# Kernel tuning notes

Measured on AMD Instinct MI355X. Metric: run time of the kernel, lower is better.

Reference implementation:

```python
import jax, jax.numpy as jnp
import numpy as np

DIM = 512
HEADS = 8
DIM_HEAD = 64
SEG = 64        # total_segment_len = segment_len + num_longterm_mem_tokens = 64
PM = 4          # num_persist_mem_tokens


def setup_inputs() -> dict:
    key = jax.random.key(0)
    ks = jax.random.split(key, 5)
    Bv, Hv, Wv = 4, 128, 128
    seq = jax.random.normal(ks[0], (Bv, Hv * Wv, DIM), jnp.float32)
    norm_w = jnp.ones((DIM,), jnp.float32)          # RMSNorm gamma
    s = DIM ** -0.5
    Wq = jax.random.normal(ks[1], (DIM, HEADS * DIM_HEAD), jnp.float32) * s
    Wkv = jax.random.normal(ks[2], (DIM, 2 * HEADS * DIM_HEAD), jnp.float32) * s
    Wo = jax.random.normal(ks[3], (HEADS * DIM_HEAD, DIM), jnp.float32) * s
    # torch inits task_memory to zeros; use small random values for a nontrivial baseline
    task_memory = jax.random.normal(ks[4], (2, HEADS, PM, DIM_HEAD), jnp.float32) * 0.02
    return {"seq": seq, "B": Bv, "H": Hv, "W": Wv, "idx": 0,
            "norm_w": norm_w, "Wq": Wq, "Wkv": Wkv, "Wo": Wo,
            "task_memory": task_memory}


def _rope(x):
    # lucidrains rotary-embedding-torch style: interleaved pairs, theta=10000
    n, d = x.shape[-2], x.shape[-1]
    inv = 1.0 / (10000.0 ** (jnp.arange(0, d, 2, dtype=jnp.float32) / d))
    fr = jnp.arange(n, dtype=jnp.float32)[:, None] * inv      # (n, d/2)
    fr = jnp.repeat(fr, 2, axis=-1)                            # (n, d) interleaved repeat
    cos, sin = jnp.cos(fr), jnp.sin(fr)
    xp = x.reshape(*x.shape[:-1], d // 2, 2)
    rot = jnp.stack((-xp[..., 1], xp[..., 0]), axis=-1).reshape(x.shape)
    return x * cos + rot * sin


def reference(seq, B, H, W, idx, norm_w, Wq, Wkv, Wo, task_memory):
    heads, dh, seg = HEADS, DIM_HEAD, SEG
    N = H * W                      # W % seg == 0 -> segmentation pad is a no-op reshape
    x = seq.reshape(B, N, DIM)
    # RMSNorm
    eps = jnp.finfo(x.dtype).eps
    x = x * jax.lax.rsqrt(jnp.mean(x * x, axis=-1, keepdims=True) + eps) * norm_w
    # cross-attention batch-half reversal trick
    x_rev = jnp.concatenate([x[B // 2:], x[:B // 2]], axis=0)
    q = x @ Wq                                  # (B, N, h*d)
    k, v = jnp.split(x_rev @ Wkv, 2, axis=-1)
    def split_heads(t):
        return t.reshape(B, N, heads, dh).transpose(0, 2, 1, 3)   # (B, h, N, d)
    q, k, v = map(split_heads, (q, k, v))
    orig_v = v
    q, k = _rope(q), _rope(k)
    # segment into windows of length seg: 'b h (w n) d -> (b w) h n d'
    w = N // seg
    def to_win(t):
        return t.reshape(B, heads, w, seg, dh).transpose(0, 2, 1, 3, 4).reshape(B * w, heads, seg, dh)
    q, k, v = map(to_win, (q, k, v))
    # prepend persistent (task) memory tokens to k/v
    pm = task_memory.shape[2]
    tmk = jnp.broadcast_to(task_memory[0], (B * w, heads, pm, dh))
    tmv = jnp.broadcast_to(task_memory[1], (B * w, heads, pm, dh))
    k = jnp.concatenate([tmk, k], axis=-2)
    v = jnp.concatenate([tmv, v], axis=-2)
    # attention within each window (non-causal, no mask)
    scores = jnp.einsum('bhid,bhjd->bhij', q, k) * (dh ** -0.5)
    attn = jax.nn.softmax(scores, axis=-1)
    out = jnp.einsum('bhij,bhjd->bhid', attn, v)
    out = out.transpose(0, 2, 1, 3).reshape(B * w, seg, heads * dh)
    out = out @ Wo
    out = out.reshape(B, w * seg, DIM)          # inverse_segment is identity (no pad)
    return out, orig_v
```

## Files before the change

kernel.cpp:

```cpp
#include <hip/hip_runtime.h>

typedef unsigned short u16;
typedef unsigned int u32;
typedef __attribute__((ext_vector_type(8))) short short8;
typedef __attribute__((ext_vector_type(4))) float f32x4;

__device__ __forceinline__ float b2f(u32 u) {
    union { u32 i; float f; } x; x.i = u << 16; return x.f;
}
__device__ __forceinline__ u16 f2b(float f) {
    union { float f; u32 i; } x; x.f = f;
    u32 u = x.i;
    u += 0x7fffu + ((u >> 16) & 1u);
    return (u16)(u >> 16);
}
__device__ __forceinline__ u32 pack2(float a, float b) {
    return (u32)f2b(a) | ((u32)f2b(b) << 16);
}
__device__ __forceinline__ void gl_lds16(const u16* g, u16* l) {
    __builtin_amdgcn_global_load_lds(
        (const __attribute__((address_space(1))) u32*)g,
        (__attribute__((address_space(3))) u32*)l, 16, 0, 0);
}

__global__ void rope_tab(float* __restrict__ cosT, float* __restrict__ sinT) {
    int idx = blockIdx.x * 256 + threadIdx.x;
    int n = idx >> 5, i = idx & 31;
    float inv = exp2f(-(float)i * 0.41524101186091903f);
    float ang = (float)n * inv;
    float s, c;
    sincosf(ang, &s, &c);
    cosT[idx] = c; sinT[idx] = s;
}

__global__ void conv_w(const float* __restrict__ Wq, const float* __restrict__ Wkv,
                       const float* __restrict__ Wo,
                       u16* __restrict__ wqkvT, u16* __restrict__ woT) {
    int idx = blockIdx.x * 256 + threadIdx.x;
    if (idx < 786432) {
        int n = idx >> 9, k = idx & 511;
        float v = (n < 512) ? Wq[k * 512 + n] : Wkv[k * 1024 + (n - 512)];
        wqkvT[idx] = f2b(v);
    } else {
        int j = idx - 786432;
        int n = j >> 9, k = j & 511;
        woT[j] = f2b(Wo[k * 512 + n]);
    }
}

__launch_bounds__(256)
__global__ void rmsnorm_k(const float* __restrict__ x, const float* __restrict__ g,
                          u16* __restrict__ xn) {
    int row  = blockIdx.x * 4 + (threadIdx.x >> 6);
    int lane = threadIdx.x & 63;
    const float4* p = (const float4*)(x + (size_t)row * 512);
    float4 a = p[lane * 2], b = p[lane * 2 + 1];
    float ss = a.x*a.x + a.y*a.y + a.z*a.z + a.w*a.w
             + b.x*b.x + b.y*b.y + b.z*b.z + b.w*b.w;
#pragma unroll
    for (int off = 1; off < 64; off <<= 1) ss += __shfl_xor(ss, off);
    float scale = rsqrtf(ss * (1.0f / 512.0f) + 1.1920929e-07f);
    const float4* gp = (const float4*)g;
    float4 g0 = gp[lane * 2], g1 = gp[lane * 2 + 1];
    uint4 u;
    u.x = pack2(a.x * scale * g0.x, a.y * scale * g0.y);
    u.y = pack2(a.z * scale * g0.z, a.w * scale * g0.w);
    u.z = pack2(b.x * scale * g1.x, b.y * scale * g1.y);
    u.w = pack2(b.z * scale * g1.z, b.w * scale * g1.w);
    *(uint4*)(xn + (size_t)row * 512 + lane * 8) = u;
}

template <int MODE>
__launch_bounds__(256)
__global__ void gemm_k512(const u16* __restrict__ A, const u16* __restrict__ Bt,
                          u16* __restrict__ oq, u16* __restrict__ ok,
                          u16* __restrict__ ov, float* __restrict__ of) {
    __shared__ u16 As[128 * 64];
    __shared__ u16 Bs[128 * 64];
    const int tid  = threadIdx.x;
    const int lane = tid & 63, w = tid >> 6;
    const int w0 = w & 1, w1 = w >> 1;
    const int l15 = lane & 15, l4 = lane >> 4;
    const int idx = blockIdx.x;
    const int xcd = idx & 7, rest = idx >> 3;
    int j, mg;
    if (MODE == 0) { j = rest % 12; mg = rest / 12; }
    else           { j = rest & 3;  mg = rest >> 2; }
    const int t0 = (mg * 8 + xcd) * 128;
    const int n0 = j * 128;
    int arow0 = t0;
    if (MODE == 0 && n0 >= 512) {
        int b = t0 >> 14;
        arow0 = (((b + 2) & 3) << 14) | (t0 & 16383);
    }
    const int lr = lane >> 3;
    const int sg = (lane & 7) ^ lr;

    f32x4 acc[4][4];
#pragma unroll
    for (int i = 0; i < 4; ++i)
#pragma unroll
        for (int jj = 0; jj < 4; ++jj) acc[i][jj] = (f32x4){0.f, 0.f, 0.f, 0.f};

    for (int kb = 0; kb < 512; kb += 64) {
        __syncthreads();
#pragma unroll
        for (int c = 0; c < 4; ++c) {
            int ca = w * 4 + c;
            int r  = ca * 8 + lr;
            gl_lds16(A  + (size_t)(arow0 + r) * 512 + kb + sg * 8, &As[ca * 512]);
            gl_lds16(Bt + (size_t)(n0    + r) * 512 + kb + sg * 8, &Bs[ca * 512]);
        }
        __syncthreads();
#pragma unroll
        for (int ksi = 0; ksi < 2; ++ksi) {
            short8 a[4], bfr[4];
#pragma unroll
            for (int mi = 0; mi < 4; ++mi) {
                int row = w0 * 64 + mi * 16 + l15;
                int ch  = (ksi * 4 + l4) ^ (row & 7);
                a[mi] = *(const short8*)&As[row * 64 + ch * 8];
            }
#pragma unroll
            for (int ni = 0; ni < 4; ++ni) {
                int row = w1 * 64 + ni * 16 + l15;
                int ch  = (ksi * 4 + l4) ^ (row & 7);
                bfr[ni] = *(const short8*)&Bs[row * 64 + ch * 8];
            }
#pragma unroll
            for (int mi = 0; mi < 4; ++mi)
#pragma unroll
                for (int ni = 0; ni < 4; ++ni)
                    acc[mi][ni] = __builtin_amdgcn_mfma_f32_16x16x32_bf16(
                        a[mi], bfr[ni], acc[mi][ni], 0, 0, 0);
        }
    }
#pragma unroll
    for (int mi = 0; mi < 4; ++mi) {
#pragma unroll
        for (int ni = 0; ni < 4; ++ni) {
#pragma unroll
            for (int r = 0; r < 4; ++r) {
                int grow = t0 + w0 * 64 + mi * 16 + l4 * 4 + r;
                int gcol = n0 + w1 * 64 + ni * 16 + l15;
                float val = acc[mi][ni][r];
                if (MODE == 1) {
                    of[(size_t)grow * 512 + gcol] = val;
                } else {
                    if (gcol < 512) {
                        oq[(size_t)grow * 512 + gcol] = f2b(val);
                    } else if (gcol < 1024) {
                        ok[(size_t)grow * 512 + (gcol - 512)] = f2b(val);
                    } else {
                        int c = gcol - 1024;
                        ov[(size_t)grow * 512 + c] = f2b(val);
                        int bb = grow >> 14, nn = grow & 16383;
                        of[((size_t)(bb * 8 + (c >> 6)) << 20) + (size_t)nn * 64 + (c & 63)] = val;
                    }
                }
            }
        }
    }
}

__launch_bounds__(256)
__global__ void attn_win(const u16* __restrict__ q_buf, const u16* __restrict__ k_buf,
                         const u16* __restrict__ v_buf, const float* __restrict__ tm,
                         const float* __restrict__ cosT, const float* __restrict__ sinT,
                         u16* __restrict__ o_buf) {
    __shared__ u16 qs[64 * 72];
    __shared__ u16 ks[80 * 72];
    __shared__ u16 vt[64 * 104];
    __shared__ u16 ps[64 * 104];
    const int tid  = threadIdx.x;
    const int lane = tid & 63, w = tid >> 6;
    const int l15 = lane & 15, l4 = lane >> 4;
    const int h = blockIdx.x, wi = blockIdx.y, b = blockIdx.z;
    const int t0 = b * 16384 + wi * 64;

    for (int i = tid; i < 896; i += 256) {
        int d = i / 14, c = i - d * 14;
        *(u32*)&vt[d * 104 + 68 + 2 * c] = 0u;
    }
    for (int i = tid; i < 432; i += 256) ((u32*)ks)[2448 + i] = 0u;

    {
        int r = tid >> 6, d = tid & 63;
        ks[r * 72 + d]   = f2b(tm[(h * 4 + r) * 64 + d]);
        vt[d * 104 + r]  = f2b(tm[2048 + (h * 4 + r) * 64 + d]);
    }
#pragma unroll
    for (int p = tid; p < 2048; p += 256) {
        int row = p >> 5, i = p & 31;
        int n = wi * 64 + row;
        float c = cosT[n * 32 + i], s = sinT[n * 32 + i];
        size_t gbase = (size_t)(t0 + row) * 512 + h * 64 + 2 * i;
        u32 qv = *(const u32*)(q_buf + gbase);
        float x0 = b2f(qv & 0xffffu), x1 = b2f(qv >> 16);
        *(u32*)&qs[row * 72 + 2 * i] = pack2(x0 * c - x1 * s, x1 * c + x0 * s);
        u32 kv = *(const u32*)(k_buf + gbase);
        x0 = b2f(kv & 0xffffu); x1 = b2f(kv >> 16);
        *(u32*)&ks[(row + 4) * 72 + 2 * i] = pack2(x0 * c - x1 * s, x1 * c + x0 * s);
    }
#pragma unroll
    for (int p = tid; p < 2048; p += 256) {
        int row = p >> 5, e = p & 31;
        u32 vv = *(const u32*)(v_buf + (size_t)(t0 + row) * 512 + h * 64 + 2 * e);
        vt[(2 * e) * 104 + 4 + row]     = (u16)(vv & 0xffffu);
        vt[(2 * e + 1) * 104 + 4 + row] = (u16)(vv >> 16);
    }
    __syncthreads();

    f32x4 sacc[5];
#pragma unroll
    for (int nt = 0; nt < 5; ++nt) sacc[nt] = (f32x4){0.f, 0.f, 0.f, 0.f};
#pragma unroll
    for (int ksi = 0; ksi < 2; ++ksi) {
        short8 a = *(const short8*)&qs[(w * 16 + l15) * 72 + ksi * 32 + l4 * 8];
#pragma unroll
        for (int nt = 0; nt < 5; ++nt) {
            short8 bfr = *(const short8*)&ks[(nt * 16 + l15) * 72 + ksi * 32 + l4 * 8];
            sacc[nt] = __builtin_amdgcn_mfma_f32_16x16x32_bf16(a, bfr, sacc[nt], 0, 0, 0);
        }
    }
    float inv_l[4];
#pragma unroll
    for (int r = 0; r < 4; ++r) {
        float sv[5];
#pragma unroll
        for (int nt = 0; nt < 5; ++nt) {
            float x = sacc[nt][r] * 0.125f;
            if (nt == 4 && l15 >= 4) x = -1e30f;
            sv[nt] = x;
        }
        float m = sv[0];
#pragma unroll
        for (int nt = 1; nt < 5; ++nt) m = fmaxf(m, sv[nt]);
#pragma unroll
        for (int off = 1; off < 16; off <<= 1) m = fmaxf(m, __shfl_xor(m, off));
        float sum = 0.f;
#pragma unroll
        for (int nt = 0; nt < 5; ++nt) { sv[nt] = __expf(sv[nt] - m); sum += sv[nt]; }
#pragma unroll
        for (int off = 1; off < 16; off <<= 1) sum += __shfl_xor(sum, off);
        inv_l[r] = 1.f / sum;
        int prow = w * 16 + l4 * 4 + r;
#pragma unroll
        for (int nt = 0; nt < 5; ++nt) ps[prow * 104 + nt * 16 + l15] = f2b(sv[nt]);
        ps[prow * 104 + 80 + l15] = 0;
    }
    __syncthreads();

    f32x4 oacc[4];
#pragma unroll
    for (int dt = 0; dt < 4; ++dt) oacc[dt] = (f32x4){0.f, 0.f, 0.f, 0.f};
#pragma unroll
    for (int ksi = 0; ksi < 3; ++ksi) {
        short8 a = *(const short8*)&ps[(w * 16 + l15) * 104 + ksi * 32 + l4 * 8];
#pragma unroll
        for (int dt = 0; dt < 4; ++dt) {
            short8 bfr = *(const short8*)&vt[(dt * 16 + l15) * 104 + ksi * 32 + l4 * 8];
            oacc[dt] = __builtin_amdgcn_mfma_f32_16x16x32_bf16(a, bfr, oacc[dt], 0, 0, 0);
        }
    }
#pragma unroll
    for (int dt = 0; dt < 4; ++dt)
#pragma unroll
        for (int r = 0; r < 4; ++r) {
            int row = w * 16 + l4 * 4 + r;
            o_buf[(size_t)(t0 + row) * 512 + h * 64 + dt * 16 + l15] =
                f2b(oacc[dt][r] * inv_l[r]);
        }
}

extern "C" void kernel_launch(void* const* d_in, const int* in_sizes, int n_in,
                              void* d_out, int out_size, void* d_ws, size_t ws_size,
                              hipStream_t stream) {
    const float* seq    = (const float*)d_in[0];
    const float* norm_w = (const float*)d_in[5];
    const float* Wq     = (const float*)d_in[6];
    const float* Wkv    = (const float*)d_in[7];
    const float* Wo     = (const float*)d_in[8];
    const float* tmem   = (const float*)d_in[9];
    float* out   = (float*)d_out;
    float* origv = out + 33554432;

    char* ws = (char*)d_ws;
    u16* xn    = (u16*)(ws);
    u16* q_buf = (u16*)(ws + 67108864);
    u16* k_buf = (u16*)(ws + 134217728);
    u16* v_buf = (u16*)(ws + 201326592);
    u16* wqkvT = (u16*)(ws + 268435456);
    u16* woT   = (u16*)(ws + 268435456 + 1572864);
    float* cosT = (float*)(ws + 270532608);
    float* sinT = cosT + 524288;

    rope_tab<<<2048, 256, 0, stream>>>(cosT, sinT);
    conv_w<<<4096, 256, 0, stream>>>(Wq, Wkv, Wo, wqkvT, woT);
    rmsnorm_k<<<16384, 256, 0, stream>>>(seq, norm_w, xn);
    gemm_k512<0><<<6144, 256, 0, stream>>>(xn, wqkvT, q_buf, k_buf, v_buf, origv);
    attn_win<<<dim3(8, 256, 4), 256, 0, stream>>>(q_buf, k_buf, v_buf, tmem, cosT, sinT, xn);
    gemm_k512<1><<<2048, 256, 0, stream>>>(xn, woT, nullptr, nullptr, nullptr, out);
}
```

Measured before the change: 701.8 us.

## Replace GEMM with 256x256 tile, 8-wave, double-buffered pipelined kernel

The 128x128 single-buffered GEMM, which synchronised on every K step, is replaced by a 256x256-tile kernel using 512 threads in 8 waves. It double-buffers LDS (64 KB per block), interleaves async global-to-LDS staging with MFMA phases, raises wave priority around MFMA blocks, and uses explicit vmcnt/lgkmcnt waits. The larger tile improves operand reuse and the pipelining hides memory latency. The costs are more barriers per iteration, heavy register use from 32 accumulators per lane, and fewer, larger blocks.

```diff
diff --git a/kernel.cpp b/kernel.cpp
--- a/kernel.cpp
+++ b/kernel.cpp
@@ -71,85 +71,149 @@
 }
 
 template <int MODE>
-__launch_bounds__(256)
-__global__ void gemm_k512(const u16* __restrict__ A, const u16* __restrict__ Bt,
-                          u16* __restrict__ oq, u16* __restrict__ ok,
-                          u16* __restrict__ ov, float* __restrict__ of) {
-    __shared__ u16 As[128 * 64];
-    __shared__ u16 Bs[128 * 64];
+__launch_bounds__(512, 2)
+__global__ void gemm8p(const u16* __restrict__ A, const u16* __restrict__ Bt,
+                       u16* __restrict__ oq, u16* __restrict__ ok,
+                       u16* __restrict__ ov, float* __restrict__ of) {
+    __shared__ u16 As[2][16384];
+    __shared__ u16 Bs[2][16384];
     const int tid  = threadIdx.x;
     const int lane = tid & 63, w = tid >> 6;
-    const int w0 = w & 1, w1 = w >> 1;
+    const int wm = w >> 2, wn = w & 3;
     const int l15 = lane & 15, l4 = lane >> 4;
+    const int lr = lane >> 3;
+    const int sg8 = (((lane & 7) ^ lr)) * 8;
+    const int bc0 = (w >> 1) * 8 + (w & 1) * 2;
+
     const int idx = blockIdx.x;
     const int xcd = idx & 7, rest = idx >> 3;
     int j, mg;
-    if (MODE == 0) { j = rest % 12; mg = rest / 12; }
-    else           { j = rest & 3;  mg = rest >> 2; }
-    const int t0 = (mg * 8 + xcd) * 128;
-    const int n0 = j * 128;
+    if (MODE == 0) { j = rest % 6; mg = rest / 6; }
+    else           { j = rest & 1; mg = rest >> 1; }
+    const int t0 = (mg * 8 + xcd) * 256;
+    const int n0 = j * 256;
     int arow0 = t0;
     if (MODE == 0 && n0 >= 512) {
         int b = t0 >> 14;
         arow0 = (((b + 2) & 3) << 14) | (t0 & 16383);
     }
-    const int lr = lane >> 3;
-    const int sg = (lane & 7) ^ lr;
-
-    f32x4 acc[4][4];
-#pragma unroll
-    for (int i = 0; i < 4; ++i)
-#pragma unroll
-        for (int jj = 0; jj < 4; ++jj) acc[i][jj] = (f32x4){0.f, 0.f, 0.f, 0.f};
-
-    for (int kb = 0; kb < 512; kb += 64) {
-        __syncthreads();
-#pragma unroll
-        for (int c = 0; c < 4; ++c) {
-            int ca = w * 4 + c;
-            int r  = ca * 8 + lr;
-            gl_lds16(A  + (size_t)(arow0 + r) * 512 + kb + sg * 8, &As[ca * 512]);
-            gl_lds16(Bt + (size_t)(n0    + r) * 512 + kb + sg * 8, &Bs[ca * 512]);
-        }
-        __syncthreads();
-#pragma unroll
-        for (int ksi = 0; ksi < 2; ++ksi) {
-            short8 a[4], bfr[4];
-#pragma unroll
-            for (int mi = 0; mi < 4; ++mi) {
-                int row = w0 * 64 + mi * 16 + l15;
-                int ch  = (ksi * 4 + l4) ^ (row & 7);
-                a[mi] = *(const short8*)&As[row * 64 + ch * 8];
-            }
-#pragma unroll
-            for (int ni = 0; ni < 4; ++ni) {
-                int row = w1 * 64 + ni * 16 + l15;
-                int ch  = (ksi * 4 + l4) ^ (row & 7);
-                bfr[ni] = *(const short8*)&Bs[row * 64 + ch * 8];
-            }
-#pragma unroll
-            for (int mi = 0; mi < 4; ++mi)
-#pragma unroll
-                for (int ni = 0; ni < 4; ++ni)
-                    acc[mi][ni] = __builtin_amdgcn_mfma_f32_16x16x32_bf16(
-                        a[mi], bfr[ni], acc[mi][ni], 0, 0, 0);
-        }
-    }
-#pragma unroll
-    for (int mi = 0; mi < 4; ++mi) {
+
+#define STAGE_A(buf, h, kt) do {                                                             \
+        int c0_ = (h) * 8 + w;                                                               \
+        gl_lds16(A + (size_t)(arow0 + c0_ * 8 + lr) * 512 + (kt) * 64 + sg8,                 \
+                 &As[buf][c0_ * 512]);                                                       \
+        int c1_ = c0_ + 16;                                                                  \
+        gl_lds16(A + (size_t)(arow0 + c1_ * 8 + lr) * 512 + (kt) * 64 + sg8,                 \
+                 &As[buf][c1_ * 512]);                                                       \
+    } while (0)
+#define STAGE_B(buf, h, kt) do {                                                             \
+        int c0_ = bc0 + (h) * 4;                                                             \
+        gl_lds16(Bt + (size_t)(n0 + c0_ * 8 + lr) * 512 + (kt) * 64 + sg8,                   \
+                 &Bs[buf][c0_ * 512]);                                                       \
+        int c1_ = c0_ + 1;                                                                   \
+        gl_lds16(Bt + (size_t)(n0 + c1_ * 8 + lr) * 512 + (kt) * 64 + sg8,                   \
+                 &Bs[buf][c1_ * 512]);                                                       \
+    } while (0)
+#define LDA(rb, mh) do {                                                                     \
+        _Pragma("unroll") for (int mi_ = 0; mi_ < 4; ++mi_) {                                \
+            int row_ = wm * 128 + ((mh) * 4 + mi_) * 16 + l15;                               \
+            _Pragma("unroll") for (int ks_ = 0; ks_ < 2; ++ks_) {                            \
+                int ch_ = (ks_ * 4 + l4) ^ (row_ & 7);                                       \
+                aF[mi_][ks_] = *(const short8*)&As[rb][row_ * 64 + ch_ * 8];                 \
+            } } } while (0)
+#define LDB(rb, nh) do {                                                                     \
+        _Pragma("unroll") for (int ni_ = 0; ni_ < 2; ++ni_) {                                \
+            int row_ = wn * 64 + ((nh) * 2 + ni_) * 16 + l15;                                \
+            _Pragma("unroll") for (int ks_ = 0; ks_ < 2; ++ks_) {                            \
+                int ch_ = (ks_ * 4 + l4) ^ (row_ & 7);                                       \
+                bF[(nh) * 2 + ni_][ks_] = *(const short8*)&Bs[rb][row_ * 64 + ch_ * 8];      \
+            } } } while (0)
+#define MMA(mh, nh) do {                                                                     \
+        _Pragma("unroll") for (int mi_ = 0; mi_ < 4; ++mi_)                                  \
+        _Pragma("unroll") for (int ni_ = 0; ni_ < 2; ++ni_)                                  \
+        _Pragma("unroll") for (int ks_ = 0; ks_ < 2; ++ks_)                                  \
+            acc[(mh) * 4 + mi_][(nh) * 2 + ni_] = __builtin_amdgcn_mfma_f32_16x16x32_bf16(   \
+                aF[mi_][ks_], bF[(nh) * 2 + ni_][ks_],                                       \
+                acc[(mh) * 4 + mi_][(nh) * 2 + ni_], 0, 0, 0);                               \
+    } while (0)
+#define BARR() do { __builtin_amdgcn_s_barrier(); __builtin_amdgcn_sched_barrier(0); } while (0)
+#define LGKM0() do { asm volatile("s_waitcnt lgkmcnt(0)" ::: "memory");                      \
+                     __builtin_amdgcn_sched_barrier(0); } while (0)
+
+    f32x4 acc[8][4];
+#pragma unroll
+    for (int mi = 0; mi < 8; ++mi)
+#pragma unroll
+        for (int ni = 0; ni < 4; ++ni) acc[mi][ni] = (f32x4){0.f, 0.f, 0.f, 0.f};
+    short8 aF[4][2], bF[4][2];
+
+    STAGE_A(0, 0, 0); STAGE_A(0, 1, 0); STAGE_B(0, 0, 0); STAGE_B(0, 1, 0);
+    STAGE_A(1, 0, 1); STAGE_B(1, 0, 1); STAGE_B(1, 1, 1);
+    asm volatile("s_waitcnt vmcnt(0)" ::: "memory");
+    __builtin_amdgcn_s_barrier();
+    __builtin_amdgcn_sched_barrier(0);
+
+    for (int i = 0; i < 4; ++i) {
+        const int kt2 = 2 * i + 2, kt3 = 2 * i + 3;
+        const bool st = (i < 3);
+        LDA(0, 0); LDB(0, 0);
+        STAGE_A(1, 1, 2 * i + 1);
+        BARR(); LGKM0();
+        __builtin_amdgcn_s_setprio(1); MMA(0, 0); __builtin_amdgcn_s_setprio(0);
+        BARR();
+        LDB(0, 1);
+        if (st) STAGE_A(0, 0, kt2);
+        BARR(); LGKM0();
+        __builtin_amdgcn_s_setprio(1); MMA(0, 1); __builtin_amdgcn_s_setprio(0);
+        BARR();
+        LDA(0, 1);
+        if (st) STAGE_B(0, 0, kt2);
+        BARR(); LGKM0();
+        __builtin_amdgcn_s_setprio(1); MMA(1, 0); __builtin_amdgcn_s_setprio(0);
+        BARR();
+        if (st) STAGE_B(0, 1, kt2);
+        BARR(); LGKM0();
+        __builtin_amdgcn_s_setprio(1); MMA(1, 1); __builtin_amdgcn_s_setprio(0);
+        if (st) { asm volatile("s_waitcnt vmcnt(6)" ::: "memory"); }
+        else    { asm volatile("s_waitcnt vmcnt(0)" ::: "memory"); }
+        BARR();
+        LDA(1, 0); LDB(1, 0);
+        if (st) STAGE_A(0, 1, kt2);
+        BARR(); LGKM0();
+        __builtin_amdgcn_s_setprio(1); MMA(0, 0); __builtin_amdgcn_s_setprio(0);
+        BARR();
+        LDB(1, 1);
+        if (st) STAGE_A(1, 0, kt3);
+        BARR(); LGKM0();
+        __builtin_amdgcn_s_setprio(1); MMA(0, 1); __builtin_amdgcn_s_setprio(0);
+        BARR();
+        LDA(1, 1);
+        if (st) STAGE_B(1, 0, kt3);
+        BARR(); LGKM0();
+        __builtin_amdgcn_s_setprio(1); MMA(1, 0); __builtin_amdgcn_s_setprio(0);
+        BARR();
+        if (st) STAGE_B(1, 1, kt3);
+        BARR(); LGKM0();
+        __builtin_amdgcn_s_setprio(1); MMA(1, 1); __builtin_amdgcn_s_setprio(0);
+        asm volatile("s_waitcnt vmcnt(6)" ::: "memory");
+        BARR();
+    }
+
+#pragma unroll
+    for (int mi = 0; mi < 8; ++mi) {
 #pragma unroll
         for (int ni = 0; ni < 4; ++ni) {
 #pragma unroll
             for (int r = 0; r < 4; ++r) {
-                int grow = t0 + w0 * 64 + mi * 16 + l4 * 4 + r;
-                int gcol = n0 + w1 * 64 + ni * 16 + l15;
+                int grow = t0 + wm * 128 + mi * 16 + l4 * 4 + r;
+                int gcol = n0 + wn * 64 + ni * 16 + l15;
                 float val = acc[mi][ni][r];
                 if (MODE == 1) {
                     of[(size_t)grow * 512 + gcol] = val;
                 } else {
-                    if (gcol < 512) {
+                    if (n0 < 512) {
                         oq[(size_t)grow * 512 + gcol] = f2b(val);
-                    } else if (gcol < 1024) {
+                    } else if (n0 < 1024) {
                         ok[(size_t)grow * 512 + (gcol - 512)] = f2b(val);
                     } else {
                         int c = gcol - 1024;
@@ -161,6 +225,13 @@
             }
         }
     }
+#undef STAGE_A
+#undef STAGE_B
+#undef LDA
+#undef LDB
+#undef MMA
+#undef BARR
+#undef LGKM0
 }
 
 __launch_bounds__(256)
@@ -298,7 +369,7 @@
     rope_tab<<<2048, 256, 0, stream>>>(cosT, sinT);
     conv_w<<<4096, 256, 0, stream>>>(Wq, Wkv, Wo, wqkvT, woT);
     rmsnorm_k<<<16384, 256, 0, stream>>>(seq, norm_w, xn);
-    gemm_k512<0><<<6144, 256, 0, stream>>>(xn, wqkvT, q_buf, k_buf, v_buf, origv);
+    gemm8p<0><<<1536, 512, 0, stream>>>(xn, wqkvT, q_buf, k_buf, v_buf, origv);
     attn_win<<<dim3(8, 256, 4), 256, 0, stream>>>(q_buf, k_buf, v_buf, tmem, cosT, sinT, xn);
-    gemm_k512<1><<<2048, 256, 0, stream>>>(xn, woT, nullptr, nullptr, nullptr, out);
-}
+    gemm8p<1><<<512, 512, 0, stream>>>(xn, woT, nullptr, nullptr, nullptr, out);
+}
```

Measured after the change: 685.1 us. 2.4% less time.

## Double-buffer LDS in GEMM kernels with async prefetch and inline ds_read

Applied to the files above, without the earlier changes.

Replaces the single-buffered GEMM with a double-buffered version. The global-to-LDS loads for tile k+2 are issued while MFMAs on the current tile run, controlled by explicit vmcnt/lgkmcnt waits, sched barriers and raised wave priority. LDS fragment reads use precomputed base addresses with inline-asm ds_read_b128 immediate offsets, and the QKV epilogue branch now keys on the block's n0 rather than the per-element column. The goal is to hide global load latency and cut address arithmetic in the two projection GEMMs, at the cost of twice the LDS per block (64KB) and hand-tuned wait counts.

```diff
diff --git a/kernel.cpp b/kernel.cpp
--- a/kernel.cpp
+++ b/kernel.cpp
@@ -21,6 +21,17 @@
     __builtin_amdgcn_global_load_lds(
         (const __attribute__((address_space(1))) u32*)g,
         (__attribute__((address_space(3))) u32*)l, 16, 0, 0);
+}
+#define DSR_C(O) else if constexpr (OFF == O) \
+    asm volatile("ds_read_b128 %0, %1 offset:" #O : "=v"(r) : "v"(b))
+template <int OFF>
+__device__ __forceinline__ short8 dsr(u32 b) {
+    short8 r;
+    if constexpr (OFF == 0) asm volatile("ds_read_b128 %0, %1" : "=v"(r) : "v"(b));
+    DSR_C(2048); DSR_C(4096); DSR_C(6144);
+    DSR_C(16384); DSR_C(18432); DSR_C(20480); DSR_C(22528);
+    else asm volatile("ds_read_b128 %0, %1" : "=v"(r) : "v"(b + OFF));
+    return r;
 }
 
 __global__ void rope_tab(float* __restrict__ cosT, float* __restrict__ sinT) {
@@ -71,16 +82,28 @@
 }
 
 template <int MODE>
-__launch_bounds__(256)
-__global__ void gemm_k512(const u16* __restrict__ A, const u16* __restrict__ Bt,
-                          u16* __restrict__ oq, u16* __restrict__ ok,
-                          u16* __restrict__ ov, float* __restrict__ of) {
-    __shared__ u16 As[128 * 64];
-    __shared__ u16 Bs[128 * 64];
+__launch_bounds__(256, 2)
+__global__ void gemm_db(const u16* __restrict__ A, const u16* __restrict__ Bt,
+                        u16* __restrict__ oq, u16* __restrict__ ok,
+                        u16* __restrict__ ov, float* __restrict__ of) {
+    __shared__ u16 As[2][8192];
+    __shared__ u16 Bs[2][8192];
     const int tid  = threadIdx.x;
     const int lane = tid & 63, w = tid >> 6;
     const int w0 = w & 1, w1 = w >> 1;
     const int l15 = lane & 15, l4 = lane >> 4;
+    const int lr = lane >> 3;
+    const int sg8 = ((lane & 7) ^ lr) * 8;
+
+    const u32 asb = (u32)(uintptr_t)&As[0][0];
+    const u32 bsb = (u32)(uintptr_t)&Bs[0][0];
+    const int chx0 = l4 ^ (l15 & 7);
+    const int chx1 = (4 + l4) ^ (l15 & 7);
+    const u32 aB0 = asb + (u32)((w0 * 64 + l15) * 128 + chx0 * 16);
+    const u32 aB1 = asb + (u32)((w0 * 64 + l15) * 128 + chx1 * 16);
+    const u32 bB0 = bsb + (u32)((w1 * 64 + l15) * 128 + chx0 * 16);
+    const u32 bB1 = bsb + (u32)((w1 * 64 + l15) * 128 + chx1 * 16);
+
     const int idx = blockIdx.x;
     const int xcd = idx & 7, rest = idx >> 3;
     int j, mg;
@@ -93,48 +116,56 @@
         int b = t0 >> 14;
         arow0 = (((b + 2) & 3) << 14) | (t0 & 16383);
     }
-    const int lr = lane >> 3;
-    const int sg = (lane & 7) ^ lr;
+
+#define STAGE(buf, kt) do {                                                                  \
+        _Pragma("unroll") for (int c_ = 0; c_ < 4; ++c_) {                                   \
+            int ca_ = w * 4 + c_;                                                            \
+            gl_lds16(A  + (size_t)(arow0 + ca_ * 8 + lr) * 512 + (kt) * 64 + sg8,            \
+                     &As[buf][ca_ * 512]);                                                   \
+            gl_lds16(Bt + (size_t)(n0    + ca_ * 8 + lr) * 512 + (kt) * 64 + sg8,            \
+                     &Bs[buf][ca_ * 512]);                                                   \
+        } } while (0)
+#define LDT(rb) do {                                                                         \
+        aF[0][0] = dsr<(rb) * 16384 +    0>(aB0); aF[0][1] = dsr<(rb) * 16384 +    0>(aB1);  \
+        aF[1][0] = dsr<(rb) * 16384 + 2048>(aB0); aF[1][1] = dsr<(rb) * 16384 + 2048>(aB1);  \
+        aF[2][0] = dsr<(rb) * 16384 + 4096>(aB0); aF[2][1] = dsr<(rb) * 16384 + 4096>(aB1);  \
+        aF[3][0] = dsr<(rb) * 16384 + 6144>(aB0); aF[3][1] = dsr<(rb) * 16384 + 6144>(aB1);  \
+        bF[0][0] = dsr<(rb) * 16384 +    0>(bB0); bF[0][1] = dsr<(rb) * 16384 +    0>(bB1);  \
+        bF[1][0] = dsr<(rb) * 16384 + 2048>(bB0); bF[1][1] = dsr<(rb) * 16384 + 2048>(bB1);  \
+        bF[2][0] = dsr<(rb) * 16384 + 4096>(bB0); bF[2][1] = dsr<(rb) * 16384 + 4096>(bB1);  \
+        bF[3][0] = dsr<(rb) * 16384 + 6144>(bB0); bF[3][1] = dsr<(rb) * 16384 + 6144>(bB1);  \
+    } while (0)
+#define MMA() do {                                                                           \
+        _Pragma("unroll") for (int mi_ = 0; mi_ < 4; ++mi_)                                  \
+        _Pragma("unroll") for (int ni_ = 0; ni_ < 4; ++ni_)                                  \
+        _Pragma("unroll") for (int ks_ = 0; ks_ < 2; ++ks_)                                  \
+            acc[mi_][ni_] = __builtin_amdgcn_mfma_f32_16x16x32_bf16(                         \
+                aF[mi_][ks_], bF[ni_][ks_], acc[mi_][ni_], 0, 0, 0);                         \
+    } while (0)
+#define TILE(kt, rb, WC) do {                                                                \
+        asm volatile("s_waitcnt vmcnt(" #WC ")" ::: "memory");                               \
+        __builtin_amdgcn_sched_barrier(0);                                                   \
+        __builtin_amdgcn_s_barrier();                                                        \
+        LDT(rb);                                                                             \
+        asm volatile("s_waitcnt lgkmcnt(0)" ::: "memory");                                   \
+        __builtin_amdgcn_sched_barrier(0);                                                   \
+        __builtin_amdgcn_s_barrier();                                                        \
+        if ((kt) < 6) STAGE(rb, (kt) + 2);                                                   \
+        __builtin_amdgcn_sched_barrier(0);                                                   \
+        __builtin_amdgcn_s_setprio(1); MMA(); __builtin_amdgcn_s_setprio(0);                 \
+    } while (0)
 
     f32x4 acc[4][4];
 #pragma unroll
-    for (int i = 0; i < 4; ++i)
-#pragma unroll
-        for (int jj = 0; jj < 4; ++jj) acc[i][jj] = (f32x4){0.f, 0.f, 0.f, 0.f};
-
-    for (int kb = 0; kb < 512; kb += 64) {
-        __syncthreads();
-#pragma unroll
-        for (int c = 0; c < 4; ++c) {
-            int ca = w * 4 + c;
-            int r  = ca * 8 + lr;
-            gl_lds16(A  + (size_t)(arow0 + r) * 512 + kb + sg * 8, &As[ca * 512]);
-            gl_lds16(Bt + (size_t)(n0    + r) * 512 + kb + sg * 8, &Bs[ca * 512]);
-        }
-        __syncthreads();
-#pragma unroll
-        for (int ksi = 0; ksi < 2; ++ksi) {
-            short8 a[4], bfr[4];
-#pragma unroll
-            for (int mi = 0; mi < 4; ++mi) {
-                int row = w0 * 64 + mi * 16 + l15;
-                int ch  = (ksi * 4 + l4) ^ (row & 7);
-                a[mi] = *(const short8*)&As[row * 64 + ch * 8];
-            }
-#pragma unroll
-            for (int ni = 0; ni < 4; ++ni) {
-                int row = w1 * 64 + ni * 16 + l15;
-                int ch  = (ksi * 4 + l4) ^ (row & 7);
-                bfr[ni] = *(const short8*)&Bs[row * 64 + ch * 8];
-            }
-#pragma unroll
-            for (int mi = 0; mi < 4; ++mi)
-#pragma unroll
-                for (int ni = 0; ni < 4; ++ni)
-                    acc[mi][ni] = __builtin_amdgcn_mfma_f32_16x16x32_bf16(
-                        a[mi], bfr[ni], acc[mi][ni], 0, 0, 0);
-        }
-    }
+    for (int mi = 0; mi < 4; ++mi)
+#pragma unroll
+        for (int ni = 0; ni < 4; ++ni) acc[mi][ni] = (f32x4){0.f, 0.f, 0.f, 0.f};
+    short8 aF[4][2], bF[4][2];
+
+    STAGE(0, 0); STAGE(1, 1);
+    TILE(0, 0, 8); TILE(1, 1, 8); TILE(2, 0, 8); TILE(3, 1, 8);
+    TILE(4, 0, 8); TILE(5, 1, 8); TILE(6, 0, 8); TILE(7, 1, 0);
+
 #pragma unroll
     for (int mi = 0; mi < 4; ++mi) {
 #pragma unroll
@@ -147,9 +178,9 @@
                 if (MODE == 1) {
                     of[(size_t)grow * 512 + gcol] = val;
                 } else {
-                    if (gcol < 512) {
+                    if (n0 < 512) {
                         oq[(size_t)grow * 512 + gcol] = f2b(val);
-                    } else if (gcol < 1024) {
+                    } else if (n0 < 1024) {
                         ok[(size_t)grow * 512 + (gcol - 512)] = f2b(val);
                     } else {
                         int c = gcol - 1024;
@@ -161,6 +192,10 @@
             }
         }
     }
+#undef STAGE
+#undef LDT
+#undef MMA
+#undef TILE
 }
 
 __launch_bounds__(256)
@@ -298,7 +333,7 @@
     rope_tab<<<2048, 256, 0, stream>>>(cosT, sinT);
     conv_w<<<4096, 256, 0, stream>>>(Wq, Wkv, Wo, wqkvT, woT);
     rmsnorm_k<<<16384, 256, 0, stream>>>(seq, norm_w, xn);
-    gemm_k512<0><<<6144, 256, 0, stream>>>(xn, wqkvT, q_buf, k_buf, v_buf, origv);
+    gemm_db<0><<<6144, 256, 0, stream>>>(xn, wqkvT, q_buf, k_buf, v_buf, origv);
     attn_win<<<dim3(8, 256, 4), 256, 0, stream>>>(q_buf, k_buf, v_buf, tmem, cosT, sinT, xn);
-    gemm_k512<1><<<2048, 256, 0, stream>>>(xn, woT, nullptr, nullptr, nullptr, out);
-}
+    gemm_db<1><<<2048, 256, 0, stream>>>(xn, woT, nullptr, nullptr, nullptr, out);
+}
```

Result: faster. 664.3 us (-5.4%).
